# Kernel tuning notes

Measured on AMD Instinct MI355X. Metric: run time of the kernel, lower is better.

Reference implementation:

```python
import jax, jax.numpy as jnp
import numpy as np
import math

N, M, EDGE_DIM, NODE_DIM, ORIG_DIM = 10000, 32, 256, 256, 256


def setup_inputs() -> dict:
    key = jax.random.key(0)
    k1, k2, k3, k4, k5, k6 = jax.random.split(key, 6)
    node_feature = jax.random.normal(k1, (N, NODE_DIM), dtype=jnp.float32)
    agg_feature = jax.random.normal(k2, (N, EDGE_DIM), dtype=jnp.float32)
    nb_id = jax.random.randint(k3, (N, M), 0, N)
    pad = jax.random.uniform(k4, (N, M)) < 0.1
    nb_id = jnp.where(pad, -1, nb_id).astype(jnp.int64)
    # attr_decoder params: Linear(node_dim + edge_dim, orig_dim)
    fan_in = NODE_DIM + EDGE_DIM
    bound = 1.0 / math.sqrt(fan_in)
    W = jax.random.uniform(k5, (fan_in, ORIG_DIM), minval=-bound, maxval=bound, dtype=jnp.float32)
    b = jax.random.uniform(k6, (ORIG_DIM,), minval=-bound, maxval=bound, dtype=jnp.float32)
    return {"node_feature": node_feature, "agg_feature": agg_feature, "nb_id": nb_id, "W": W, "b": b}


def reference(node_feature, agg_feature, nb_id, W, b):
    n, d = agg_feature.shape
    # -1 sentinel -> row n of [agg_feature; zeros] (matches torch negative indexing into the cat)
    idx = jnp.where(nb_id < 0, n, nb_id)
    padded = jnp.concatenate([agg_feature, jnp.zeros((1, d), agg_feature.dtype)], axis=0)
    nb_feature = padded[idx]                                  # [N, M, d]
    score = jnp.einsum('nd,nmd->nm', agg_feature, nb_feature)  # [N, M]
    score = jnp.where(nb_id == -1, jnp.asarray(-1e10, score.dtype), score)
    attn = jax.nn.softmax(score / math.sqrt(d), axis=-1)       # masked-fill BEFORE scaling, as in source
    context = jnp.einsum('nm,nmd->nd', attn, nb_feature)       # [N, d]
    h = jnp.concatenate([node_feature, context], axis=-1)      # [N, node_dim + edge_dim]
    decode_attribute = jax.nn.sigmoid(h @ W + b)               # [N, orig_dim]
    decode_adj = jax.nn.sigmoid(agg_feature @ agg_feature.T)   # [N, N]
    return decode_attribute, decode_adj
```

## Files before the change

kernel.cpp:

```cpp
#include <hip/hip_runtime.h>
#include <hip/hip_fp16.h>
#include <cstdint>
#include <cstddef>

#define NNODES 10000
#define DIM 256
#define MNB 32
#define NT 79
#define NTRI (NT*(NT+1)/2)

typedef __attribute__((ext_vector_type(8))) _Float16 f16x8;
typedef __attribute__((ext_vector_type(4))) float f32x4;

__device__ inline unsigned short f16_rne(float f) {
    return __half_as_ushort(__float2half(f));
}
__device__ inline float f16_to_f32(unsigned short h) {
    return __half2float(__ushort_as_half(h));
}

__global__ __launch_bounds__(256) void split2_kernel(
    const float* __restrict__ in0, const float* __restrict__ in1,
    unsigned short* __restrict__ hi0, unsigned short* __restrict__ lo0,
    unsigned short* __restrict__ hi1, unsigned short* __restrict__ lo1,
    int count8)
{
    const int i = blockIdx.x * 256 + threadIdx.x;
    if (i >= count8) return;
    const float* in = blockIdx.y ? in1 : in0;
    unsigned short* hi = blockIdx.y ? hi1 : hi0;
    unsigned short* lo = blockIdx.y ? lo1 : lo0;
    float4 a = ((const float4*)in)[i * 2];
    float4 b = ((const float4*)in)[i * 2 + 1];
    float f[8] = {a.x, a.y, a.z, a.w, b.x, b.y, b.z, b.w};
    unsigned int hp[4], lp[4];
    #pragma unroll
    for (int j = 0; j < 4; ++j) {
        unsigned short h0 = f16_rne(f[2 * j]);
        unsigned short h1 = f16_rne(f[2 * j + 1]);
        unsigned short l0 = f16_rne(f[2 * j]     - f16_to_f32(h0));
        unsigned short l1 = f16_rne(f[2 * j + 1] - f16_to_f32(h1));
        hp[j] = (unsigned int)h0 | ((unsigned int)h1 << 16);
        lp[j] = (unsigned int)l0 | ((unsigned int)l1 << 16);
    }
    ((uint4*)hi)[i] = make_uint4(hp[0], hp[1], hp[2], hp[3]);
    ((uint4*)lo)[i] = make_uint4(lp[0], lp[1], lp[2], lp[3]);
}

__global__ __launch_bounds__(256) void wt_split_kernel(
    const float* __restrict__ W,
    unsigned short* __restrict__ wth,
    unsigned short* __restrict__ wtl)
{
    const int r = blockIdx.x;
    const int t = threadIdx.x;
    #pragma unroll
    for (int h = 0; h < 2; ++h) {
        const int k = h * 256 + t;
        float v = W[(size_t)k * DIM + r];
        unsigned short hh = f16_rne(v);
        unsigned short ll = f16_rne(v - f16_to_f32(hh));
        wth[(size_t)r * 512 + k] = hh;
        wtl[(size_t)r * 512 + k] = ll;
    }
}

__global__ __launch_bounds__(256) void attn_ctx_kernel(
    const unsigned short* __restrict__ aggh,
    const int* __restrict__ nb_id,
    unsigned short* __restrict__ ctxh)
{
    const int n = blockIdx.x;
    const int t = threadIdx.x;
    __shared__ uint2 s_nb[MNB][64];
    __shared__ float s_score[MNB];
    __shared__ int   s_idx[MNB];

    if (t < MNB) s_idx[t] = nb_id[n * MNB + t];
    __syncthreads();

    const int wave = t >> 6;
    const int lane = t & 63;

    const uint2 q = ((const uint2*)aggh)[(size_t)n * 64 + lane];
    float qf[4];
    qf[0] = f16_to_f32((unsigned short)(q.x & 0xffff));
    qf[1] = f16_to_f32((unsigned short)(q.x >> 16));
    qf[2] = f16_to_f32((unsigned short)(q.y & 0xffff));
    qf[3] = f16_to_f32((unsigned short)(q.y >> 16));

    #pragma unroll
    for (int mi = 0; mi < 8; ++mi) {
        const int m = wave * 8 + mi;
        const int idx = s_idx[m];
        uint2 v = make_uint2(0u, 0u);
        if (idx >= 0) v = ((const uint2*)aggh)[(size_t)idx * 64 + lane];
        s_nb[m][lane] = v;
        float p = qf[0] * f16_to_f32((unsigned short)(v.x & 0xffff))
                + qf[1] * f16_to_f32((unsigned short)(v.x >> 16))
                + qf[2] * f16_to_f32((unsigned short)(v.y & 0xffff))
                + qf[3] * f16_to_f32((unsigned short)(v.y >> 16));
        #pragma unroll
        for (int off = 32; off; off >>= 1) p += __shfl_down(p, off);
        if (lane == 0) s_score[m] = (idx >= 0) ? p * (1.f / 16.f) : -6.25e8f;
    }
    __syncthreads();

    float mx = -INFINITY;
    #pragma unroll
    for (int m = 0; m < MNB; ++m) mx = fmaxf(mx, s_score[m]);
    float wgt[MNB];
    float denom = 0.f;
    #pragma unroll
    for (int m = 0; m < MNB; ++m) { wgt[m] = __expf(s_score[m] - mx); denom += wgt[m]; }
    const float inv = 1.f / denom;

    const __half* nbf = (const __half*)s_nb;
    float c = 0.f;
    #pragma unroll
    for (int m = 0; m < MNB; ++m)
        c = fmaf(wgt[m] * inv, __half2float(nbf[m * DIM + t]), c);

    ctxh[(size_t)n * DIM + t] = f16_rne(c);
}

#define LDS_AH 0
#define LDS_BH 16384
#define LDS_BL 32768

__global__ __launch_bounds__(256, 3) void attr_mfma_kernel(
    const unsigned short* __restrict__ nodeh,
    const unsigned short* __restrict__ ctxh,
    const unsigned short* __restrict__ wth,
    const unsigned short* __restrict__ wtl,
    const float* __restrict__ bias,
    float* __restrict__ out)
{
    const int bj = blockIdx.x;
    const int bi = blockIdx.y;

    __shared__ __align__(16) char lds[49152];

    const int t = threadIdx.x;
    const int l = t & 63;
    const int w = t >> 6;
    const int wm = w >> 1;
    const int wn = w & 1;

    const int srow = t >> 1;
    const int shalf = t & 1;
    const int rowA = min(bi * 128 + srow, NNODES - 1);
    const size_t offA = (size_t)rowA * DIM;
    const int rowB = bj * 128 + srow;
    const size_t offB = (size_t)rowB * 512;

    f32x4 acc[4][4] = {};

    for (int kb = 0; kb < 512; kb += 64) {
        const unsigned short* aH = (kb < 256) ? nodeh : ctxh;
        const int koff = kb & 255;
        __syncthreads();
        #pragma unroll
        for (int c = 0; c < 4; ++c) {
            const int k8 = shalf * 4 + c;
            const int chp = k8 ^ (srow & 7);
            uint4 vah = *(const uint4*)&aH[offA + koff + k8 * 8];
            uint4 vbh = *(const uint4*)&wth[offB + kb + k8 * 8];
            uint4 vbl = *(const uint4*)&wtl[offB + kb + k8 * 8];
            *(uint4*)&lds[LDS_AH + srow * 128 + chp * 16] = vah;
            *(uint4*)&lds[LDS_BH + srow * 128 + chp * 16] = vbh;
            *(uint4*)&lds[LDS_BL + srow * 128 + chp * 16] = vbl;
        }
        __syncthreads();

        #pragma unroll
        for (int s = 0; s < 2; ++s) {
            f16x8 ah[4], bh[4], bl[4];
            #pragma unroll
            for (int m = 0; m < 4; ++m) {
                const int ra = wm * 64 + m * 16 + (l & 15);
                const int ca = (s * 4 + (l >> 4)) ^ (ra & 7);
                ah[m] = *(const f16x8*)&lds[LDS_AH + ra * 128 + ca * 16];
                const int rb = wn * 64 + m * 16 + (l & 15);
                const int cb = (s * 4 + (l >> 4)) ^ (rb & 7);
                bh[m] = *(const f16x8*)&lds[LDS_BH + rb * 128 + cb * 16];
                bl[m] = *(const f16x8*)&lds[LDS_BL + rb * 128 + cb * 16];
            }
            #pragma unroll
            for (int m = 0; m < 4; ++m)
                #pragma unroll
                for (int n = 0; n < 4; ++n) {
                    acc[m][n] = __builtin_amdgcn_mfma_f32_16x16x32_f16(ah[m], bh[n], acc[m][n], 0, 0, 0);
                    acc[m][n] = __builtin_amdgcn_mfma_f32_16x16x32_f16(ah[m], bl[n], acc[m][n], 0, 0, 0);
                }
        }
    }

    float bias_v[4];
    #pragma unroll
    for (int n = 0; n < 4; ++n)
        bias_v[n] = bias[bj * 128 + wn * 64 + n * 16 + (l & 15)];
    #pragma unroll
    for (int m = 0; m < 4; ++m)
        #pragma unroll
        for (int n = 0; n < 4; ++n)
            #pragma unroll
            for (int j = 0; j < 4; ++j)
                acc[m][n][j] = 1.f / (1.f + __expf(-(acc[m][n][j] + bias_v[n])));

    float* sf = (float*)lds;
    #pragma unroll
    for (int half = 0; half < 2; ++half) {
        __syncthreads();
        if (wm == half) {
            #pragma unroll
            for (int m = 0; m < 4; ++m)
                #pragma unroll
                for (int n = 0; n < 4; ++n)
                    #pragma unroll
                    for (int j = 0; j < 4; ++j) {
                        const int r = m * 16 + (l >> 4) * 4 + j;
                        const int c = wn * 64 + n * 16 + (l & 15);
                        sf[r * 128 + c] = acc[m][n][j];
                    }
        }
        __syncthreads();
        const int c4 = t & 31;
        const int gc = bj * 128 + c4 * 4;
        #pragma unroll
        for (int it = 0; it < 8; ++it) {
            const int r = it * 8 + (t >> 5);
            const int gr = bi * 128 + half * 64 + r;
            if (gr < NNODES) {
                float4 v = *(float4*)&sf[r * 128 + c4 * 4];
                *(float4*)&out[(size_t)gr * DIM + gc] = v;
            }
        }
    }
}

__global__ __launch_bounds__(256, 3) void adj_mfma_kernel(
    const unsigned short* __restrict__ aggh,
    const unsigned short* __restrict__ aggl,
    float* __restrict__ out)
{
    const int tid = blockIdx.x;
    int bi = (int)((2 * NT + 1 - sqrtf((float)((2 * NT + 1) * (2 * NT + 1)) - 8.0f * (float)tid)) * 0.5f);
    while (bi > 0 && bi * NT - bi * (bi - 1) / 2 > tid) --bi;
    while ((bi + 1) * NT - (bi + 1) * bi / 2 <= tid) ++bi;
    const int bj = bi + (tid - (bi * NT - bi * (bi - 1) / 2));

    __shared__ __align__(16) char lds[49152];

    const int t = threadIdx.x;
    const int l = t & 63;
    const int w = t >> 6;
    const int wm = w >> 1;
    const int wn = w & 1;

    const int srow = t >> 1;
    const int shalf = t & 1;
    const int rowA = min(bi * 128 + srow, NNODES - 1);
    const int rowB = min(bj * 128 + srow, NNODES - 1);
    const size_t offA = (size_t)rowA * DIM;
    const size_t offB = (size_t)rowB * DIM;

    f32x4 acc[4][4] = {};

    for (int kb = 0; kb < DIM; kb += 64) {
        __syncthreads();
        #pragma unroll
        for (int c = 0; c < 4; ++c) {
            const int k8 = shalf * 4 + c;
            const int chp = k8 ^ (srow & 7);
            uint4 vah = *(const uint4*)&aggh[offA + kb + k8 * 8];
            uint4 vbh = *(const uint4*)&aggh[offB + kb + k8 * 8];
            uint4 vbl = *(const uint4*)&aggl[offB + kb + k8 * 8];
            *(uint4*)&lds[LDS_AH + srow * 128 + chp * 16] = vah;
            *(uint4*)&lds[LDS_BH + srow * 128 + chp * 16] = vbh;
            *(uint4*)&lds[LDS_BL + srow * 128 + chp * 16] = vbl;
        }
        __syncthreads();

        #pragma unroll
        for (int s = 0; s < 2; ++s) {
            f16x8 ah[4], bh[4], bl[4];
            #pragma unroll
            for (int m = 0; m < 4; ++m) {
                const int ra = wm * 64 + m * 16 + (l & 15);
                const int ca = (s * 4 + (l >> 4)) ^ (ra & 7);
                ah[m] = *(const f16x8*)&lds[LDS_AH + ra * 128 + ca * 16];
                const int rb = wn * 64 + m * 16 + (l & 15);
                const int cb = (s * 4 + (l >> 4)) ^ (rb & 7);
                bh[m] = *(const f16x8*)&lds[LDS_BH + rb * 128 + cb * 16];
                bl[m] = *(const f16x8*)&lds[LDS_BL + rb * 128 + cb * 16];
            }
            #pragma unroll
            for (int m = 0; m < 4; ++m)
                #pragma unroll
                for (int n = 0; n < 4; ++n) {
                    acc[m][n] = __builtin_amdgcn_mfma_f32_16x16x32_f16(ah[m], bh[n], acc[m][n], 0, 0, 0);
                    acc[m][n] = __builtin_amdgcn_mfma_f32_16x16x32_f16(ah[m], bl[n], acc[m][n], 0, 0, 0);
                }
        }
    }

    #pragma unroll
    for (int m = 0; m < 4; ++m)
        #pragma unroll
        for (int n = 0; n < 4; ++n)
            #pragma unroll
            for (int j = 0; j < 4; ++j)
                acc[m][n][j] = 1.f / (1.f + __expf(-acc[m][n][j]));

    float* sf = (float*)lds;
    const size_t NN = NNODES;

    #pragma unroll
    for (int half = 0; half < 2; ++half) {
        __syncthreads();
        if (wm == half) {
            #pragma unroll
            for (int m = 0; m < 4; ++m)
                #pragma unroll
                for (int n = 0; n < 4; ++n)
                    #pragma unroll
                    for (int j = 0; j < 4; ++j) {
                        const int r = m * 16 + (l >> 4) * 4 + j;
                        const int c = wn * 64 + n * 16 + (l & 15);
                        sf[r * 128 + c] = acc[m][n][j];
                    }
        }
        __syncthreads();
        const int c4 = t & 31;
        const int gc = bj * 128 + c4 * 4;
        #pragma unroll
        for (int it = 0; it < 8; ++it) {
            const int r = it * 8 + (t >> 5);
            const int gr = bi * 128 + half * 64 + r;
            if (gr < NNODES && gc < NNODES) {
                f32x4 v = *(f32x4*)&sf[r * 128 + c4 * 4];
                __builtin_nontemporal_store(v, (f32x4*)&out[(size_t)gr * NN + gc]);
            }
        }
    }

    if (bi != bj) {
        #pragma unroll
        for (int half = 0; half < 2; ++half) {
            __syncthreads();
            if (wn == half) {
                #pragma unroll
                for (int m = 0; m < 4; ++m)
                    #pragma unroll
                    for (int n = 0; n < 4; ++n)
                        #pragma unroll
                        for (int j = 0; j < 4; ++j) {
                            const int r = wm * 64 + m * 16 + (l >> 4) * 4 + j;
                            const int c = n * 16 + (l & 15);
                            sf[c * 128 + (((r >> 2) ^ (c & 7)) << 2) + (r & 3)] = acc[m][n][j];
                        }
            }
            __syncthreads();
            const int g = t & 31;
            const int gc2 = bi * 128 + g * 4;
            #pragma unroll
            for (int it = 0; it < 8; ++it) {
                const int rt = it * 8 + (t >> 5);
                const int gr2 = bj * 128 + half * 64 + rt;
                if (gr2 < NNODES) {
                    f32x4 v = *(f32x4*)&sf[rt * 128 + ((g ^ (rt & 7)) << 2)];
                    __builtin_nontemporal_store(v, (f32x4*)&out[(size_t)gr2 * NN + gc2]);
                }
            }
        }
    }
}

extern "C" void kernel_launch(void* const* d_in, const int* in_sizes, int n_in,
                              void* d_out, int out_size, void* d_ws, size_t ws_size,
                              hipStream_t stream) {
    const float* node = (const float*)d_in[0];
    const float* agg  = (const float*)d_in[1];
    const int*   nb   = (const int*)d_in[2];
    const float* W    = (const float*)d_in[3];
    const float* bias = (const float*)d_in[4];

    float* out_attr = (float*)d_out;
    float* out_adj  = (float*)d_out + (size_t)NNODES * DIM;

    char* ws = (char*)d_ws;
    unsigned short* aggh  = (unsigned short*)(ws);
    unsigned short* aggl  = (unsigned short*)(ws + 5120000);
    unsigned short* nodeh = (unsigned short*)(ws + 10240000);
    unsigned short* nodel = (unsigned short*)(ws + 15360000);
    unsigned short* ctxh  = (unsigned short*)(ws + 20480000);
    unsigned short* wth   = (unsigned short*)(ws + 25600000);
    unsigned short* wtl   = (unsigned short*)(ws + 26124288);

    const int count8 = NNODES * DIM / 8;
    dim3 gs((count8 + 255) / 256, 2);
    split2_kernel<<<gs, 256, 0, stream>>>(agg, node, aggh, aggl, nodeh, nodel, count8);

    adj_mfma_kernel<<<NTRI, 256, 0, stream>>>(aggh, aggl, out_adj);

    wt_split_kernel<<<256, 256, 0, stream>>>(W, wth, wtl);
    attn_ctx_kernel<<<NNODES, 256, 0, stream>>>(aggh, nb, ctxh);

    dim3 g2(2, NT);
    attr_mfma_kernel<<<g2, 256, 0, stream>>>(nodeh, ctxh, wth, wtl, bias, out_attr);
}
```

Baseline: 190.5 us.

## Merge split kernels into one pre-pass, drop node low part, use normal stores

Combines the fp16 hi/lo split of agg/node and the W transpose-split into one launch, which removes a kernel launch. It also stops computing and writing the low-order half of node_feature, because the attribute GEMM only reads nodeh. The adjacency output stores switch from nontemporal stores to regular stores. The store change alters cache behaviour on a 400MB output write and could help or hurt.

Measured after the change: 211.5 us. 1.11x slower.

```diff
diff --git a/kernel.cpp b/kernel.cpp
--- a/kernel.cpp
+++ b/kernel.cpp
@@ -19,49 +19,54 @@
     return __half2float(__ushort_as_half(h));
 }
 
-__global__ __launch_bounds__(256) void split2_kernel(
-    const float* __restrict__ in0, const float* __restrict__ in1,
-    unsigned short* __restrict__ hi0, unsigned short* __restrict__ lo0,
-    unsigned short* __restrict__ hi1, unsigned short* __restrict__ lo1,
-    int count8)
+__global__ __launch_bounds__(256) void pre_kernel(
+    const float* __restrict__ agg, const float* __restrict__ node,
+    const float* __restrict__ W,
+    unsigned short* __restrict__ aggh, unsigned short* __restrict__ aggl,
+    unsigned short* __restrict__ nodeh,
+    unsigned short* __restrict__ wth, unsigned short* __restrict__ wtl)
 {
-    const int i = blockIdx.x * 256 + threadIdx.x;
-    if (i >= count8) return;
-    const float* in = blockIdx.y ? in1 : in0;
-    unsigned short* hi = blockIdx.y ? hi1 : hi0;
-    unsigned short* lo = blockIdx.y ? lo1 : lo0;
-    float4 a = ((const float4*)in)[i * 2];
-    float4 b = ((const float4*)in)[i * 2 + 1];
-    float f[8] = {a.x, a.y, a.z, a.w, b.x, b.y, b.z, b.w};
-    unsigned int hp[4], lp[4];
-    #pragma unroll
-    for (int j = 0; j < 4; ++j) {
-        unsigned short h0 = f16_rne(f[2 * j]);
-        unsigned short h1 = f16_rne(f[2 * j + 1]);
-        unsigned short l0 = f16_rne(f[2 * j]     - f16_to_f32(h0));
-        unsigned short l1 = f16_rne(f[2 * j + 1] - f16_to_f32(h1));
-        hp[j] = (unsigned int)h0 | ((unsigned int)h1 << 16);
-        lp[j] = (unsigned int)l0 | ((unsigned int)l1 << 16);
-    }
-    ((uint4*)hi)[i] = make_uint4(hp[0], hp[1], hp[2], hp[3]);
-    ((uint4*)lo)[i] = make_uint4(lp[0], lp[1], lp[2], lp[3]);
-}
-
-__global__ __launch_bounds__(256) void wt_split_kernel(
-    const float* __restrict__ W,
-    unsigned short* __restrict__ wth,
-    unsigned short* __restrict__ wtl)
-{
-    const int r = blockIdx.x;
+    const int bx = blockIdx.x;
     const int t = threadIdx.x;
-    #pragma unroll
-    for (int h = 0; h < 2; ++h) {
-        const int k = h * 256 + t;
-        float v = W[(size_t)k * DIM + r];
-        unsigned short hh = f16_rne(v);
-        unsigned short ll = f16_rne(v - f16_to_f32(hh));
-        wth[(size_t)r * 512 + k] = hh;
-        wtl[(size_t)r * 512 + k] = ll;
+    const int count8 = NNODES * DIM / 8;
+
+    if (bx < 2500) {
+        const int which = bx >= 1250;
+        const int i = (which ? bx - 1250 : bx) * 256 + t;
+        if (i >= count8) return;
+        const float* in = which ? node : agg;
+        float4 a = ((const float4*)in)[i * 2];
+        float4 b = ((const float4*)in)[i * 2 + 1];
+        float f[8] = {a.x, a.y, a.z, a.w, b.x, b.y, b.z, b.w};
+        unsigned int hp[4], lp[4];
+        #pragma unroll
+        for (int j = 0; j < 4; ++j) {
+            unsigned short h0 = f16_rne(f[2 * j]);
+            unsigned short h1 = f16_rne(f[2 * j + 1]);
+            hp[j] = (unsigned int)h0 | ((unsigned int)h1 << 16);
+            if (!which) {
+                unsigned short l0 = f16_rne(f[2 * j]     - f16_to_f32(h0));
+                unsigned short l1 = f16_rne(f[2 * j + 1] - f16_to_f32(h1));
+                lp[j] = (unsigned int)l0 | ((unsigned int)l1 << 16);
+            }
+        }
+        if (which) {
+            ((uint4*)nodeh)[i] = make_uint4(hp[0], hp[1], hp[2], hp[3]);
+        } else {
+            ((uint4*)aggh)[i] = make_uint4(hp[0], hp[1], hp[2], hp[3]);
+            ((uint4*)aggl)[i] = make_uint4(lp[0], lp[1], lp[2], lp[3]);
+        }
+    } else {
+        const int r = bx - 2500;
+        #pragma unroll
+        for (int h = 0; h < 2; ++h) {
+            const int k = h * 256 + t;
+            float v = W[(size_t)k * DIM + r];
+            unsigned short hh = f16_rne(v);
+            unsigned short ll = f16_rne(v - f16_to_f32(hh));
+            wth[(size_t)r * 512 + k] = hh;
+            wtl[(size_t)r * 512 + k] = ll;
+        }
     }
 }
 
@@ -340,7 +345,7 @@
             const int gr = bi * 128 + half * 64 + r;
             if (gr < NNODES && gc < NNODES) {
                 f32x4 v = *(f32x4*)&sf[r * 128 + c4 * 4];
-                __builtin_nontemporal_store(v, (f32x4*)&out[(size_t)gr * NN + gc]);
+                *(f32x4*)&out[(size_t)gr * NN + gc] = v;
             }
         }
     }
@@ -370,7 +375,7 @@
                 const int gr2 = bj * 128 + half * 64 + rt;
                 if (gr2 < NNODES) {
                     f32x4 v = *(f32x4*)&sf[rt * 128 + ((g ^ (rt & 7)) << 2)];
-                    __builtin_nontemporal_store(v, (f32x4*)&out[(size_t)gr2 * NN + gc2]);
+                    *(f32x4*)&out[(size_t)gr2 * NN + gc2] = v;
                 }
             }
         }
@@ -393,18 +398,14 @@
     unsigned short* aggh  = (unsigned short*)(ws);
     unsigned short* aggl  = (unsigned short*)(ws + 5120000);
     unsigned short* nodeh = (unsigned short*)(ws + 10240000);
-    unsigned short* nodel = (unsigned short*)(ws + 15360000);
-    unsigned short* ctxh  = (unsigned short*)(ws + 20480000);
-    unsigned short* wth   = (unsigned short*)(ws + 25600000);
-    unsigned short* wtl   = (unsigned short*)(ws + 26124288);
-
-    const int count8 = NNODES * DIM / 8;
-    dim3 gs((count8 + 255) / 256, 2);
-    split2_kernel<<<gs, 256, 0, stream>>>(agg, node, aggh, aggl, nodeh, nodel, count8);
+    unsigned short* ctxh  = (unsigned short*)(ws + 15360000);
+    unsigned short* wth   = (unsigned short*)(ws + 20480000);
+    unsigned short* wtl   = (unsigned short*)(ws + 21004288);
+
+    pre_kernel<<<2756, 256, 0, stream>>>(agg, node, W, aggh, aggl, nodeh, wth, wtl);
 
     adj_mfma_kernel<<<NTRI, 256, 0, stream>>>(aggh, aggl, out_adj);
 
-    wt_split_kernel<<<256, 256, 0, stream>>>(W, wth, wtl);
     attn_ctx_kernel<<<NNODES, 256, 0, stream>>>(aggh, nb, ctxh);
 
     dim3 g2(2, NT);
```
